# Kernel optimization log

Measured on AMD Instinct MI355X. Metric: run time of the kernel, lower is better.

## Reference

```python
import jax, jax.numpy as jnp
import numpy as np

B, NPG, F, DEG = 512, 512, 255, 32   # graphs, nodes-per-graph, feat dim, avg degree
N = B * NPG
E = N * DEG
RATIO = 0.5
K = int(np.ceil(RATIO * NPG))        # nodes kept per graph (static)


def setup_inputs() -> dict:
    key = jax.random.key(0)
    k1, k2, k3, k4, k5 = jax.random.split(key, 5)
    out = jax.random.normal(k1, (N, F), jnp.float32)
    z = jax.random.randint(k2, (N,), 0, 101)  # z == 100 marks virtual nodes
    # random edges strictly within each graph (block-contiguous node ids)
    local = jax.random.randint(k3, (2, B, NPG * DEG), 0, NPG)
    offs = (jnp.arange(B) * NPG)[None, :, None]
    edge_index = (local + offs).reshape(2, E)
    batch = jnp.repeat(jnp.arange(B), NPG)
    W = jax.random.normal(k4, (F + 1, 1), jnp.float32) * (1.0 / np.sqrt(F + 1))
    b = jnp.zeros((1,), jnp.float32)
    edge_attr = jax.random.normal(k5, (E, 1), jnp.float32)  # carried but unused by SAGPool scoring
    return dict(out=out, z=z, edge_index=edge_index, batch=batch, W=W, b=b,
                edge_attr=edge_attr)


def gcn_score(x, edge_index, W, b):
    """GCNConv(F+1 -> 1) with self-loops and symmetric normalization."""
    n = x.shape[0]
    h = (x @ W)[:, 0]  # [N] since out_channels == 1
    row, col = edge_index[0], edge_index[1]
    loop = jnp.arange(n)
    row = jnp.concatenate([row, loop])
    col = jnp.concatenate([col, loop])
    deg = jax.ops.segment_sum(jnp.ones_like(col, x.dtype), col, num_segments=n)
    dinv = jnp.where(deg > 0, jax.lax.rsqrt(deg), 0.0)
    norm = dinv[row] * dinv[col]  # deg^-1/2 * deg^-1/2 per edge
    agg = jax.ops.segment_sum(norm * h[row], col, num_segments=n)
    return agg + b[0]


def reference(out, z, edge_index, batch, W, b, edge_attr):
    # concat real/virtual bit
    real = (z != 100).astype(out.dtype)[:, None]
    x = jnp.concatenate([out, real], axis=-1)          # [N, F+1]
    # SAGPooling: score nodes, tanh nonlinearity
    score = jnp.tanh(gcn_score(x, edge_index, W, b))   # [N]
    # per-graph top-k (uniform graph size -> static-shape top_k)
    sv, si = jax.lax.top_k(score.reshape(B, NPG), K)   # [B, K]
    perm = (si + (jnp.arange(B) * NPG)[:, None]).reshape(-1)  # global node ids
    xp = x[perm] * sv.reshape(-1)[:, None]             # gated selected nodes [B*K, F+1]
    # global_mean_pool over pooled batch (k nodes per graph)
    return xp.reshape(B, K, F + 1).mean(axis=1)        # [B, F+1]
```

## Files before the change

### kernel.cpp

```cpp
#include <hip/hip_runtime.h>
#include <math.h>

#define NPG     512
#define B_GR    512
#define FDIM    255
#define DEG     32
#define EPG     (NPG * DEG)
#define N_NODES (B_GR * NPG)
#define E_TOT   (N_NODES * DEG)
#define K_KEEP  256

#define CH_NODES 16
#define CH_FLOATS (CH_NODES * FDIM)
#define CH_F4     (CH_FLOATS / 4)
#define NCHUNK    (NPG / CH_NODES)

__device__ __forceinline__ void lds_dma16(const void* g, void* l) {
    __builtin_amdgcn_global_load_lds(
        (const __attribute__((address_space(1))) unsigned int*)g,
        (__attribute__((address_space(3))) unsigned int*)l, 16, 0, 0);
}

__global__ __launch_bounds__(1024, 8) void k_fused(const float* __restrict__ feat,
                                                   const int*   __restrict__ z,
                                                   const int*   __restrict__ ei,
                                                   const float* __restrict__ W,
                                                   const float* __restrict__ bias,
                                                   float*       __restrict__ outp) {
    __shared__ __align__(16) float stage[2][CH_FLOATS];
    __shared__ __align__(16) float Wl[256];
    __shared__ __align__(16) float score[NPG];
    __shared__ float h_l[NPG];
    __shared__ float dinv_l[NPG];
    __shared__ float agg[NPG];
    __shared__ float realb[NPG];
    __shared__ int   deg[NPG];
    __shared__ int   rank2[2][NPG];
    __shared__ int   selidx[K_KEEP];
    __shared__ float selsc[K_KEEP];
    __shared__ float red[3][256];
    __shared__ int   cnt;

    const int g     = blockIdx.x;
    const int tid   = threadIdx.x;
    const int nbase = g * NPG;
    const int lane  = tid & 63;
    const int wave  = tid >> 6;

    const int4* colp4 = (const int4*)(ei + (size_t)E_TOT + (size_t)g * EPG);
    const int4* rowp4 = (const int4*)(ei + (size_t)g * EPG);

    if (tid < 256) Wl[tid] = W[tid];
    if (tid < NPG) {
        realb[tid] = (z[nbase + tid] != 100) ? 1.f : 0.f;
        deg[tid]   = 1;
    }
    if (tid == 0) cnt = 0;
    __syncthreads();

    {
        const float w0   = Wl[lane];
        const float w64  = Wl[lane + 64];
        const float w128 = Wl[lane + 128];
        const float w192 = (lane < 63) ? Wl[lane + 192] : 0.f;
        const float w255 = Wl[FDIM];
        const char* srcb = (const char*)(feat + (size_t)nbase * FDIM);

        if (tid < CH_F4)
            lds_dma16(srcb + (size_t)tid * 16, (char*)stage[0] + (size_t)tid * 16);
        asm volatile("s_waitcnt vmcnt(0)" ::: "memory");
        __builtin_amdgcn_s_barrier();
        __builtin_amdgcn_sched_barrier(0);

        for (int ch = 0; ch < NCHUNK; ++ch) {
            const float* cur = stage[ch & 1];
            float*       nxt = (float*)stage[(ch & 1) ^ 1];

            int4 c4;
            const bool do_deg = ((ch & 7) == 0);
            if (do_deg)
                c4 = colp4[(ch >> 3) * 1024 + tid];

            if (ch + 1 < NCHUNK && tid < CH_F4)
                lds_dma16(srcb + (size_t)(ch + 1) * 16320 + (size_t)tid * 16,
                          (char*)nxt + (size_t)tid * 16);

            const float* row = cur + wave * FDIM;
            float acc = (lane == 0) ? realb[ch * CH_NODES + wave] * w255 : 0.f;
            acc = fmaf(row[lane],       w0,   acc);
            acc = fmaf(row[lane + 64],  w64,  acc);
            acc = fmaf(row[lane + 128], w128, acc);
            if (lane < 63)
                acc = fmaf(row[lane + 192], w192, acc);
#pragma unroll
            for (int off = 32; off; off >>= 1)
                acc += __shfl_down(acc, off, 64);
            if (lane == 0) h_l[ch * CH_NODES + wave] = acc;

            if (do_deg) {
                atomicAdd(&deg[c4.x - nbase], 1);
                atomicAdd(&deg[c4.y - nbase], 1);
                atomicAdd(&deg[c4.z - nbase], 1);
                atomicAdd(&deg[c4.w - nbase], 1);
            }

            asm volatile("s_waitcnt vmcnt(0)" ::: "memory");
            __builtin_amdgcn_s_barrier();
            __builtin_amdgcn_sched_barrier(0);
        }
    }
    __syncthreads();

    if (tid < NPG) {
        const float di = (float)(1.0 / sqrt((double)deg[tid]));
        dinv_l[tid] = di;
        const float v = di * h_l[tid];
        h_l[tid] = v;
        agg[tid] = v;
    }
    __syncthreads();

#pragma unroll
    for (int it = 0; it < 4; ++it) {
        const int  idx = it * 1024 + tid;
        const int4 r4  = rowp4[idx];
        const int4 c4  = colp4[idx];
        atomicAdd(&agg[c4.x - nbase], h_l[r4.x - nbase]);
        atomicAdd(&agg[c4.y - nbase], h_l[r4.y - nbase]);
        atomicAdd(&agg[c4.z - nbase], h_l[r4.z - nbase]);
        atomicAdd(&agg[c4.w - nbase], h_l[r4.w - nbase]);
    }
    __syncthreads();

    if (tid < NPG)
        score[tid] = tanhf(fmaf(agg[tid], dinv_l[tid], bias[0]));
    __syncthreads();

    {
        const int    node = tid & (NPG - 1);
        const int    half = tid >> 9;
        const float  sc   = score[node];
        const float4* s4p = (const float4*)&score[half * 256];
        int part = 0;
#pragma unroll 8
        for (int i = 0; i < 64; ++i) {
            const float4 s4 = s4p[i];
            const int    j  = half * 256 + i * 4;
            part += (s4.x > sc) || (s4.x == sc && (j + 0) < node);
            part += (s4.y > sc) || (s4.y == sc && (j + 1) < node);
            part += (s4.z > sc) || (s4.z == sc && (j + 2) < node);
            part += (s4.w > sc) || (s4.w == sc && (j + 3) < node);
        }
        rank2[half][node] = part;
    }
    __syncthreads();

    if (tid < NPG) {
        const int rank = rank2[0][tid] + rank2[1][tid];
        if (rank < K_KEEP) {
            const int slot = atomicAdd(&cnt, 1);
            selidx[slot] = tid;
            selsc[slot]  = score[tid];
        }
    }
    __syncthreads();

    {
        const int f = tid & 255;
        const int q = tid >> 8;
        float acc = 0.f;
        if (f < FDIM) {
            const float* fb = feat + (size_t)nbase * FDIM + f;
#pragma unroll
            for (int k = 0; k < 64; k += 8) {
                int   is[8]; float ss[8]; float tv[8];
#pragma unroll
                for (int j = 0; j < 8; ++j) {
                    is[j] = selidx[q + 4 * (k + j)];
                    ss[j] = selsc [q + 4 * (k + j)];
                }
#pragma unroll
                for (int j = 0; j < 8; ++j)
                    tv[j] = fb[(size_t)is[j] * FDIM];
#pragma unroll
                for (int j = 0; j < 8; ++j)
                    acc = fmaf(ss[j], tv[j], acc);
            }
        } else {
            for (int s = q; s < K_KEEP; s += 4)
                acc = fmaf(selsc[s], realb[selidx[s]], acc);
        }
        if (q) red[q - 1][f] = acc;
        __syncthreads();
        if (q == 0)
            outp[(size_t)g * 256 + f] =
                (acc + red[0][f] + red[1][f] + red[2][f]) * (1.f / K_KEEP);
    }
}

extern "C" void kernel_launch(void* const* d_in, const int* in_sizes, int n_in,
                              void* d_out, int out_size, void* d_ws, size_t ws_size,
                              hipStream_t stream) {
    const float* feat = (const float*)d_in[0];
    const int*   z    = (const int*)  d_in[1];
    const int*   ei   = (const int*)  d_in[2];
    const float* W    = (const float*)d_in[4];
    const float* bias = (const float*)d_in[5];
    float* outp = (float*)d_out;

    k_fused<<<B_GR, 1024, 0, stream>>>(feat, z, ei, W, bias, outp);
}
```

Measured before the change: 124.5 us.

## Triple-buffer feature staging and cache edge columns in LDS as ushort

The feature staging moves from double to triple buffering with a prefetch distance of two, so each chunk waits only for the older DMA (vmcnt(1)) rather than draining all loads. Degree counting leaves the feature loop and becomes a separate phase that reads the column indices once, converts them to 16-bit local ids and stores them in the now-free staging LDS. The aggregation phase then reuses those LDS ids instead of reading the columns from global memory a second time. The extra staging buffer raises LDS use, and the launch-bounds occupancy hint is dropped, which may lower blocks per CU.

```diff
diff --git a/kernel.cpp b/kernel.cpp
--- a/kernel.cpp
+++ b/kernel.cpp
@@ -21,16 +21,16 @@
         (__attribute__((address_space(3))) unsigned int*)l, 16, 0, 0);
 }
 
-__global__ __launch_bounds__(1024, 8) void k_fused(const float* __restrict__ feat,
-                                                   const int*   __restrict__ z,
-                                                   const int*   __restrict__ ei,
-                                                   const float* __restrict__ W,
-                                                   const float* __restrict__ bias,
-                                                   float*       __restrict__ outp) {
-    __shared__ __align__(16) float stage[2][CH_FLOATS];
+__global__ __launch_bounds__(1024) void k_fused(const float* __restrict__ feat,
+                                                const int*   __restrict__ z,
+                                                const int*   __restrict__ ei,
+                                                const float* __restrict__ W,
+                                                const float* __restrict__ bias,
+                                                float*       __restrict__ outp) {
+    __shared__ __align__(16) float stage[3][CH_FLOATS];
     __shared__ __align__(16) float Wl[256];
     __shared__ __align__(16) float score[NPG];
-    __shared__ float h_l[NPG];
+    __shared__ float v_l[NPG];
     __shared__ float dinv_l[NPG];
     __shared__ float agg[NPG];
     __shared__ float realb[NPG];
@@ -66,26 +66,26 @@
         const float w255 = Wl[FDIM];
         const char* srcb = (const char*)(feat + (size_t)nbase * FDIM);
 
-        if (tid < CH_F4)
-            lds_dma16(srcb + (size_t)tid * 16, (char*)stage[0] + (size_t)tid * 16);
-        asm volatile("s_waitcnt vmcnt(0)" ::: "memory");
-        __builtin_amdgcn_s_barrier();
-        __builtin_amdgcn_sched_barrier(0);
+        if (tid < CH_F4) {
+            lds_dma16(srcb + (size_t)tid * 16,
+                      (char*)stage[0] + (size_t)tid * 16);
+            lds_dma16(srcb + 16320 + (size_t)tid * 16,
+                      (char*)stage[1] + (size_t)tid * 16);
+        }
 
         for (int ch = 0; ch < NCHUNK; ++ch) {
-            const float* cur = stage[ch & 1];
-            float*       nxt = (float*)stage[(ch & 1) ^ 1];
-
-            int4 c4;
-            const bool do_deg = ((ch & 7) == 0);
-            if (do_deg)
-                c4 = colp4[(ch >> 3) * 1024 + tid];
-
-            if (ch + 1 < NCHUNK && tid < CH_F4)
-                lds_dma16(srcb + (size_t)(ch + 1) * 16320 + (size_t)tid * 16,
-                          (char*)nxt + (size_t)tid * 16);
-
-            const float* row = cur + wave * FDIM;
+            if (ch == NCHUNK - 1)
+                asm volatile("s_waitcnt vmcnt(0)" ::: "memory");
+            else
+                asm volatile("s_waitcnt vmcnt(1)" ::: "memory");
+            __builtin_amdgcn_s_barrier();
+            __builtin_amdgcn_sched_barrier(0);
+
+            if (ch + 2 < NCHUNK && tid < CH_F4)
+                lds_dma16(srcb + (size_t)(ch + 2) * 16320 + (size_t)tid * 16,
+                          (char*)stage[(ch + 2) % 3] + (size_t)tid * 16);
+
+            const float* row = stage[ch % 3] + wave * FDIM;
             float acc = (lane == 0) ? realb[ch * CH_NODES + wave] * w255 : 0.f;
             acc = fmaf(row[lane],       w0,   acc);
             acc = fmaf(row[lane + 64],  w64,  acc);
@@ -95,52 +95,66 @@
 #pragma unroll
             for (int off = 32; off; off >>= 1)
                 acc += __shfl_down(acc, off, 64);
-            if (lane == 0) h_l[ch * CH_NODES + wave] = acc;
-
-            if (do_deg) {
-                atomicAdd(&deg[c4.x - nbase], 1);
-                atomicAdd(&deg[c4.y - nbase], 1);
-                atomicAdd(&deg[c4.z - nbase], 1);
-                atomicAdd(&deg[c4.w - nbase], 1);
-            }
-
-            asm volatile("s_waitcnt vmcnt(0)" ::: "memory");
-            __builtin_amdgcn_s_barrier();
-            __builtin_amdgcn_sched_barrier(0);
-        }
-    }
-    __syncthreads();
-
-    if (tid < NPG) {
-        const float di = (float)(1.0 / sqrt((double)deg[tid]));
-        dinv_l[tid] = di;
-        const float v = di * h_l[tid];
-        h_l[tid] = v;
-        agg[tid] = v;
-    }
-    __syncthreads();
-
-#pragma unroll
-    for (int it = 0; it < 4; ++it) {
-        const int  idx = it * 1024 + tid;
-        const int4 r4  = rowp4[idx];
-        const int4 c4  = colp4[idx];
-        atomicAdd(&agg[c4.x - nbase], h_l[r4.x - nbase]);
-        atomicAdd(&agg[c4.y - nbase], h_l[r4.y - nbase]);
-        atomicAdd(&agg[c4.z - nbase], h_l[r4.z - nbase]);
-        atomicAdd(&agg[c4.w - nbase], h_l[r4.w - nbase]);
-    }
-    __syncthreads();
+            if (lane == 0) v_l[ch * CH_NODES + wave] = acc;
+        }
+    }
+    __syncthreads();
+
+    {
+        ushort4* cc4 = (ushort4*)stage;
+
+        int4 c4v[4];
+#pragma unroll
+        for (int it = 0; it < 4; ++it) c4v[it] = colp4[it * 1024 + tid];
+#pragma unroll
+        for (int it = 0; it < 4; ++it) {
+            const int4 c4 = c4v[it];
+            ushort4 u;
+            u.x = (unsigned short)(c4.x - nbase);
+            u.y = (unsigned short)(c4.y - nbase);
+            u.z = (unsigned short)(c4.z - nbase);
+            u.w = (unsigned short)(c4.w - nbase);
+            cc4[it * 1024 + tid] = u;
+            atomicAdd(&deg[u.x], 1);
+            atomicAdd(&deg[u.y], 1);
+            atomicAdd(&deg[u.z], 1);
+            atomicAdd(&deg[u.w], 1);
+        }
+        __syncthreads();
+
+        if (tid < NPG) {
+            const float di = (float)(1.0 / sqrt((double)deg[tid]));
+            dinv_l[tid] = di;
+            const float v = di * v_l[tid];
+            v_l[tid] = v;
+            agg[tid] = v;
+        }
+        __syncthreads();
+
+        int4 r4v[4];
+#pragma unroll
+        for (int it = 0; it < 4; ++it) r4v[it] = rowp4[it * 1024 + tid];
+#pragma unroll
+        for (int it = 0; it < 4; ++it) {
+            const ushort4 u  = cc4[it * 1024 + tid];
+            const int4    r4 = r4v[it];
+            atomicAdd(&agg[u.x], v_l[r4.x - nbase]);
+            atomicAdd(&agg[u.y], v_l[r4.y - nbase]);
+            atomicAdd(&agg[u.z], v_l[r4.z - nbase]);
+            atomicAdd(&agg[u.w], v_l[r4.w - nbase]);
+        }
+        __syncthreads();
+    }
 
     if (tid < NPG)
         score[tid] = tanhf(fmaf(agg[tid], dinv_l[tid], bias[0]));
     __syncthreads();
 
     {
-        const int    node = tid & (NPG - 1);
-        const int    half = tid >> 9;
-        const float  sc   = score[node];
-        const float4* s4p = (const float4*)&score[half * 256];
+        const int     node = tid & (NPG - 1);
+        const int     half = tid >> 9;
+        const float   sc   = score[node];
+        const float4* s4p  = (const float4*)&score[half * 256];
         int part = 0;
 #pragma unroll 8
         for (int i = 0; i < 64; ++i) {
```

Result: no change. 123.3 us (-1.0%).
